# Optimization experiments

Hardware: AMD Instinct MI355X
Metric: run time of the kernel (lower is better)

## Reference

```python
import jax, jax.numpy as jnp
import numpy as np

LATENT_N = 1024
COMMITMENT_COST = 1.0
TEMP = 0.1


def setup_inputs() -> dict:
    key = jax.random.key(0)
    k0, k1, k2, k3, k4, k5 = jax.random.split(key, 6)
    N, D, H, Fd, K = 65536, 1024, 128, 512, LATENT_N
    input_data = jax.random.normal(k0, (N, D), dtype=jnp.float32)
    W1 = jax.random.normal(k1, (D, H), dtype=jnp.float32) * (1.0 / np.sqrt(D))
    b1 = jnp.zeros((H,), dtype=jnp.float32)
    W2 = jax.random.normal(k2, (H, Fd), dtype=jnp.float32) * (1.0 / np.sqrt(H))
    b2 = jnp.zeros((Fd,), dtype=jnp.float32)
    code_book = jax.random.uniform(k3, (K, Fd), dtype=jnp.float32,
                                   minval=-1.0 / K, maxval=1.0 / K)
    return {"input_data": input_data, "W1": W1, "b1": b1,
            "W2": W2, "b2": b2, "code_book": code_book}


def reference(input_data, W1, b1, W2, b2, code_book):
    # feat MLP: Linear -> ReLU -> Linear
    z = jnp.matmul(jnp.maximum(jnp.matmul(input_data, W1) + b1, 0.0), W2) + b2  # [N, F]
    # squared L2 distances to codebook entries: [N, K]
    distances = (jnp.sum(z * z, axis=1, keepdims=True)
                 + jnp.sum(code_book * code_book, axis=1)
                 - 2.0 * jnp.matmul(z, code_book.T))
    logits = -distances / TEMP
    # categorical sample per row (softmax of logits)
    idx = jax.random.categorical(jax.random.key(42), logits, axis=-1)  # [N] int
    encodings = jax.nn.one_hot(idx, LATENT_N, dtype=z.dtype)  # [N, K]
    quantized = jnp.matmul(encodings, code_book)  # [N, F] == code_book[idx]
    e_latent_loss = jnp.mean((jax.lax.stop_gradient(quantized) - z) ** 2)
    q_latent_loss = jnp.mean((quantized - jax.lax.stop_gradient(z)) ** 2)
    loss = q_latent_loss + COMMITMENT_COST * e_latent_loss
    # straight-through estimator
    quantized_st = z + jax.lax.stop_gradient(quantized - z)
    avg_probs = jnp.mean(encodings, axis=0)  # [K]
    perplexity = jnp.exp(-jnp.sum(avg_probs * jnp.log(avg_probs + 1e-10)))
    return (loss, quantized_st, perplexity, encodings, -distances)
```

## Files before the change

### kernel.cpp

```cpp
#include <hip/hip_runtime.h>
#include <stdint.h>

#define N_ROWS 65536
#define DIM 1024
#define HID 128
#define FD 512
#define KCB 1024
#define HALFCNT 33554432u

#define OFF_Q    1
#define OFF_PERP 33554433
#define OFF_ENC  33554434
#define OFF_ND   100663298

typedef __attribute__((ext_vector_type(8))) short sh8;
typedef __attribute__((ext_vector_type(4))) float f32x4;

__device__ __forceinline__ uint32_t rotl32(uint32_t v, int r) { return (v << r) | (v >> (32 - r)); }

__device__ __forceinline__ void threefry(uint32_t c0, uint32_t c1, uint32_t& o0, uint32_t& o1) {
    const uint32_t ks0 = 0u, ks1 = 42u, ks2 = 0x1BD11BDAu ^ 0u ^ 42u;
    uint32_t x0 = c0 + ks0, x1 = c1 + ks1;
#define TFR(r) x0 += x1; x1 = rotl32(x1, r); x1 ^= x0;
    TFR(13) TFR(15) TFR(26) TFR(6)  x0 += ks1; x1 += ks2 + 1u;
    TFR(17) TFR(29) TFR(16) TFR(24) x0 += ks2; x1 += ks0 + 2u;
    TFR(13) TFR(15) TFR(26) TFR(6)  x0 += ks0; x1 += ks1 + 3u;
    TFR(17) TFR(29) TFR(16) TFR(24) x0 += ks1; x1 += ks2 + 4u;
    TFR(13) TFR(15) TFR(26) TFR(6)  x0 += ks2; x1 += ks0 + 5u;
#undef TFR
    o0 = x0; o1 = x1;
}

__device__ __forceinline__ float gumbel_f32(uint32_t b) {
    uint32_t m = b >> 9;
    float u = m ? (float)m * 1.1920928955078125e-07f : 1.17549435e-38f;
    const float LN2 = 0.6931471805599453f;
    return -LN2 * __log2f(-LN2 * __log2f(u));
}

__device__ __forceinline__ ushort bf16rne(float f) {
    uint32_t u = __float_as_uint(f);
    return (ushort)((u + 0x7FFFu + ((u >> 16) & 1u)) >> 16);
}
__device__ __forceinline__ uint32_t pack2rne(float a, float b) {
    return (uint32_t)bf16rne(a) | ((uint32_t)bf16rne(b) << 16);
}

__device__ __forceinline__ void async_cp16(const void* g, void* l) {
    __builtin_amdgcn_global_load_lds(
        (const __attribute__((address_space(1))) void*)g,
        (__attribute__((address_space(3))) void*)l, 16, 0, 0);
}

__device__ __forceinline__ void nt_store4(float* p, float x, float y, float z, float w) {
    f32x4 v = {x, y, z, w};
    __builtin_nontemporal_store(v, (f32x4*)p);
}

__global__ __launch_bounds__(256) void k_prep(const float* __restrict__ cb, const float* __restrict__ W1,
                                              const float* __restrict__ W2,
                                              ushort* __restrict__ cbh, double* __restrict__ cc,
                                              ushort* __restrict__ w1th, ushort* __restrict__ w2th,
                                              int* __restrict__ counts, double* __restrict__ lossb,
                                              unsigned long long* __restrict__ wkey) {
    int gb = blockIdx.x, t = threadIdx.x;
    if (gb < 256) {
        int k = gb * 4 + (t >> 6), l = t & 63;
        const float4* row = (const float4*)(cb + (size_t)k * FD);
        float4 a = row[l * 2], b = row[l * 2 + 1];
        float v[8] = {a.x, a.y, a.z, a.w, b.x, b.y, b.z, b.w};
        double s = 0.0;
        uint32_t hu[4];
        #pragma unroll
        for (int e = 0; e < 4; ++e) {
            hu[e] = pack2rne(v[2 * e], v[2 * e + 1]);
            s = fma((double)v[2 * e], (double)v[2 * e], s);
            s = fma((double)v[2 * e + 1], (double)v[2 * e + 1], s);
        }
        *(uint4*)(cbh + (size_t)k * FD + l * 8) = make_uint4(hu[0], hu[1], hu[2], hu[3]);
        for (int off = 32; off; off >>= 1) s += __shfl_down(s, off, 64);
        if (l == 0) cc[k] = s;
    } else if (gb < 384) {
        int c = gb - 256;
        #pragma unroll
        for (int u = 0; u < 4; ++u) {
            int k = t + u * 256;
            w1th[(size_t)c * DIM + k] = bf16rne(W1[(size_t)k * HID + c]);
        }
    } else if (gb < 640) {
        int c = (gb - 384) * 2 + (t >> 7);
        int tt = t & 127;
        w2th[(size_t)c * HID + tt] = bf16rne(W2[(size_t)tt * FD + c]);
    } else if (gb == 640) {
        for (int k = t; k < KCB; k += 256) counts[k] = 0;
        lossb[t] = 0.0;
    } else {
        unsigned long long* p = wkey + (size_t)(gb - 641) * 2048;
        #pragma unroll
        for (int u = 0; u < 8; ++u) p[t + u * 256] = 0ull;
    }
}

__global__ __launch_bounds__(256) void kAB(const float* __restrict__ X, const ushort* __restrict__ w1th,
                                           const float* __restrict__ b1, const ushort* __restrict__ w2th,
                                           const float* __restrict__ b2,
                                           ushort* __restrict__ zbh, float* __restrict__ zz) {
    __shared__ __align__(16) char lds[24576];
    __shared__ float zzp[64][2];
    int t = threadIdx.x;
    int lane = t & 63, w = t >> 6;
    int wr = w >> 1, wc = w & 1;
    int lane15 = lane & 15, lg = lane >> 4;
    int n0 = blockIdx.x * 64;
    f32x4 zero4 = {0.f, 0.f, 0.f, 0.f};
    f32x4 acc[2][4];
    #pragma unroll
    for (int i = 0; i < 2; ++i)
        #pragma unroll
        for (int j = 0; j < 4; ++j) acc[i][j] = zero4;

    int xr = t >> 2;
    int cq = (t & 3) * 2;
    int xsw = xr & 7;

    for (int k0 = 0; k0 < DIM; k0 += 64) {
        #pragma unroll
        for (int i = 0; i < 4; ++i) {
            int rr = w * 32 + i * 8;
            int row = rr + (lane >> 3);
            int csrc = (lane & 7) ^ (row & 7);
            async_cp16(w1th + (size_t)row * DIM + k0 + csrc * 8, lds + 8192 + rr * 128);
        }
        const float* xp = X + (size_t)(n0 + xr) * DIM + k0 + cq * 8;
        #pragma unroll
        for (int c = 0; c < 2; ++c) {
            float4 a = *(const float4*)(xp + c * 8);
            float4 b = *(const float4*)(xp + c * 8 + 4);
            uint4 hv;
            hv.x = pack2rne(a.x, a.y);
            hv.y = pack2rne(a.z, a.w);
            hv.z = pack2rne(b.x, b.y);
            hv.w = pack2rne(b.z, b.w);
            *(uint4*)(lds + xr * 128 + (((cq + c) ^ xsw) << 4)) = hv;
        }
        __syncthreads();
        #pragma unroll
        for (int kh = 0; kh < 2; ++kh) {
            int ch = kh * 4 + lg;
            sh8 ah[2], bh[4];
            #pragma unroll
            for (int i = 0; i < 2; ++i) {
                int ra = wr * 32 + i * 16 + lane15;
                ah[i] = *(const sh8*)(lds + ra * 128 + ((ch ^ (ra & 7)) << 4));
            }
            #pragma unroll
            for (int j = 0; j < 4; ++j) {
                int rb = wc * 64 + j * 16 + lane15;
                bh[j] = *(const sh8*)(lds + 8192 + rb * 128 + ((ch ^ (rb & 7)) << 4));
            }
            #pragma unroll
            for (int i = 0; i < 2; ++i)
                #pragma unroll
                for (int j = 0; j < 4; ++j)
                    acc[i][j] = __builtin_amdgcn_mfma_f32_16x16x32_bf16(ah[i], bh[j], acc[i][j], 0, 0, 0);
        }
        __syncthreads();
    }
    #pragma unroll
    for (int j = 0; j < 4; ++j) {
        int hcol = wc * 64 + j * 16 + lane15;
        float b1v = b1[hcol];
        int k8 = hcol >> 3, klo = hcol & 7;
        #pragma unroll
        for (int i = 0; i < 2; ++i)
            #pragma unroll
            for (int r = 0; r < 4; ++r) {
                int row = wr * 32 + i * 16 + lg * 4 + r;
                ushort hb = bf16rne(fmaxf(acc[i][j][r] + b1v, 0.f));
                *(ushort*)(lds + row * 256 + ((k8 ^ (row & 7)) << 4) + klo * 2) = hb;
            }
    }
    __syncthreads();
    float zsum[8];
    #pragma unroll
    for (int e = 0; e < 8; ++e) zsum[e] = 0.f;
    for (int c2 = 0; c2 < 4; ++c2) {
        f32x4 acc2[2][4];
        #pragma unroll
        for (int i = 0; i < 2; ++i)
            #pragma unroll
            for (int j = 0; j < 4; ++j) acc2[i][j] = zero4;
        #pragma unroll
        for (int kh = 0; kh < 4; ++kh) {
            int ch = kh * 4 + lg;
            sh8 ah[2], bh[4];
            #pragma unroll
            for (int i = 0; i < 2; ++i) {
                int ra = wr * 32 + i * 16 + lane15;
                ah[i] = *(const sh8*)(lds + ra * 256 + ((ch ^ (ra & 7)) << 4));
            }
            #pragma unroll
            for (int j = 0; j < 4; ++j) {
                int col = c2 * 128 + wc * 64 + j * 16 + lane15;
                bh[j] = *(const sh8*)(w2th + (size_t)col * HID + ch * 8);
            }
            #pragma unroll
            for (int i = 0; i < 2; ++i)
                #pragma unroll
                for (int j = 0; j < 4; ++j)
                    acc2[i][j] = __builtin_amdgcn_mfma_f32_16x16x32_bf16(ah[i], bh[j], acc2[i][j], 0, 0, 0);
        }
        #pragma unroll
        for (int j = 0; j < 4; ++j) {
            int col = c2 * 128 + wc * 64 + j * 16 + lane15;
            float b2v = b2[col];
            #pragma unroll
            for (int i = 0; i < 2; ++i)
                #pragma unroll
                for (int r = 0; r < 4; ++r) {
                    int row = wr * 32 + i * 16 + lg * 4 + r;
                    float v = acc2[i][j][r] + b2v;
                    zbh[(size_t)(n0 + row) * FD + col] = bf16rne(v);
                    zsum[i * 4 + r] = fmaf(v, v, zsum[i * 4 + r]);
                }
        }
    }
    #pragma unroll
    for (int e = 0; e < 8; ++e) {
        float s = zsum[e];
        s += __shfl_xor(s, 1, 64); s += __shfl_xor(s, 2, 64);
        s += __shfl_xor(s, 4, 64); s += __shfl_xor(s, 8, 64);
        if (lane15 == 0) zzp[wr * 32 + (e >> 2) * 16 + lg * 4 + (e & 3)][wc] = s;
    }
    __syncthreads();
    if (t < 64) zz[n0 + t] = zzp[t][0] + zzp[t][1];
}

__global__ __launch_bounds__(256) void k_mfma3p(const ushort* __restrict__ zbh, const ushort* __restrict__ cbh,
                                                const float* __restrict__ zz, const double* __restrict__ cc,
                                                float* __restrict__ nd,
                                                unsigned long long* __restrict__ wkey) {
    __shared__ __align__(16) char lds[32768];
    int t = threadIdx.x;
    int lane = t & 63, w = t >> 6;
    int wr = w >> 1, wc = w & 1;
    int bid = blockIdx.x;
    int pm = ((bid >> 6) << 3) | (bid & 7);
    int bkn = (bid >> 3) & 7;
    const ushort* Bhg = cbh + (size_t)bkn * 128 * FD;

    f32x4 zero4 = {0.f, 0.f, 0.f, 0.f};
    f32x4 acc[4][4];
    #pragma unroll
    for (int i = 0; i < 4; ++i)
        #pragma unroll
        for (int j = 0; j < 4; ++j) acc[i][j] = zero4;

    for (int k0 = 0; k0 < FD; k0 += 64) {
        #pragma unroll
        for (int i = 0; i < 4; ++i) {
            int rr = w * 32 + i * 8;
            int row = rr + (lane >> 3);
            int csrc = (lane & 7) ^ (row & 7);
            int ga = pm * 64 + (row >> 6) * 32 + (row & 31) + (((row >> 5) & 1) ? 32768 : 0);
            async_cp16(zbh + (size_t)ga * FD + k0 + csrc * 8, lds + rr * 128);
            async_cp16(Bhg + (size_t)row * FD + k0 + csrc * 8, lds + 16384 + rr * 128);
        }
        __syncthreads();
        #pragma unroll
        for (int kh = 0; kh < 2; ++kh) {
            int ch = kh * 4 + (lane >> 4);
            sh8 ah[4], bh[4];
            #pragma unroll
            for (int i = 0; i < 4; ++i) {
                int ra = wr * 64 + i * 16 + (lane & 15);
                ah[i] = *(const sh8*)(lds + ra * 128 + ((ch ^ (ra & 7)) << 4));
            }
            #pragma unroll
            for (int j = 0; j < 4; ++j) {
                int rb = wc * 64 + j * 16 + (lane & 15);
                bh[j] = *(const sh8*)(lds + 16384 + rb * 128 + ((ch ^ (rb & 7)) << 4));
            }
            #pragma unroll
            for (int i = 0; i < 4; ++i)
                #pragma unroll
                for (int j = 0; j < 4; ++j)
                    acc[i][j] = __builtin_amdgcn_mfma_f32_16x16x32_bf16(ah[i], bh[j], acc[i][j], 0, 0, 0);
        }
        __syncthreads();
    }
    int lane15 = lane & 15, lg = lane >> 4;
    int gcol[4];
    double ccv[4];
    #pragma unroll
    for (int j = 0; j < 4; ++j) {
        gcol[j] = bkn * 128 + wc * 64 + j * 16 + lane15;
        ccv[j] = cc[gcol[j]];
    }
    #pragma unroll
    for (int i2 = 0; i2 < 2; ++i2)
        #pragma unroll
        for (int r = 0; r < 4; ++r) {
            int lowrow = pm * 64 + wr * 32 + i2 * 16 + lg * 4 + r;
            int hirow  = lowrow + 32768;
            float zlo = zz[lowrow], zhi = zz[hirow];
            double zvl = (double)zlo, zvh = (double)zhi;
            size_t rofl = (size_t)lowrow << 10;
            size_t rofh = (size_t)hirow << 10;
            unsigned long long bkl = 0ull, bkh = 0ull;
            #pragma unroll
            for (int j = 0; j < 4; ++j) {
                float ndl = (float)(2.0 * (double)acc[i2][j][r] - zvl - ccv[j]);
                float ndh = (float)(2.0 * (double)acc[i2 + 2][j][r] - zvh - ccv[j]);
                __builtin_nontemporal_store(ndl, nd + rofl + gcol[j]);
                __builtin_nontemporal_store(ndh, nd + rofh + gcol[j]);
                uint32_t base = (uint32_t)lowrow * 1024u + (uint32_t)gcol[j];
                uint32_t r0, r1;
                threefry(base, base + HALFCNT, r0, r1);
                float sl = (ndl + zlo) * 10.0f + gumbel_f32(r0);
                float sh = (ndh + zhi) * 10.0f + gumbel_f32(r1);
                uint32_t ul = __float_as_uint(sl);
                ul ^= (uint32_t)(((int32_t)ul >> 31) | 0x80000000);
                uint32_t uh = __float_as_uint(sh);
                uh ^= (uint32_t)(((int32_t)uh >> 31) | 0x80000000);
                unsigned long long kl = ((unsigned long long)ul << 32) | (uint32_t)(1023 - gcol[j]);
                unsigned long long kh2 = ((unsigned long long)uh << 32) | (uint32_t)(1023 - gcol[j]);
                if (kl > bkl) bkl = kl;
                if (kh2 > bkh) bkh = kh2;
            }
            #pragma unroll
            for (int m = 1; m <= 8; m <<= 1) {
                unsigned long long ol = __shfl_xor(bkl, m, 64);
                unsigned long long oh = __shfl_xor(bkh, m, 64);
                if (ol > bkl) bkl = ol;
                if (oh > bkh) bkh = oh;
            }
            if (lane15 == 0) {
                atomicMax(&wkey[lowrow], bkl);
                atomicMax(&wkey[hirow], bkh);
            }
        }
}

__global__ __launch_bounds__(256) void k_enc2(const unsigned long long* __restrict__ wkey,
                                              const float* __restrict__ nd, const float* __restrict__ cb,
                                              float* __restrict__ enc, float* __restrict__ qz,
                                              int* __restrict__ counts, double* __restrict__ lossb) {
    int t = threadIdx.x;
    int n0 = blockIdx.x * 16;
    __shared__ int si[16];
    if (t < 16) {
        int n = n0 + t;
        unsigned long long best = wkey[n];
        int k = 1023 - (int)(best & 0xFFFFFFFFull);
        si[t] = k;
        atomicAdd(&counts[k], 1);
        float ndv = nd[(size_t)n * KCB + k];
        atomicAdd(&lossb[n & 255], -(double)ndv);
    }
    __syncthreads();
    #pragma unroll
    for (int r = 0; r < 16; ++r) {
        int id = si[r];
        int base = t * 4;
        nt_store4(&enc[(size_t)(n0 + r) * KCB + base],
                  (id == base)     ? 1.0f : 0.0f,
                  (id == base + 1) ? 1.0f : 0.0f,
                  (id == base + 2) ? 1.0f : 0.0f,
                  (id == base + 3) ? 1.0f : 0.0f);
    }
    for (int e = t; e < 16 * 128; e += 256) {
        int r = e >> 7, s = e & 127;
        float4 v = *(const float4*)&cb[(size_t)si[r] * FD + s * 4];
        nt_store4(&qz[(size_t)(n0 + r) * FD + s * 4], v.x, v.y, v.z, v.w);
    }
}

__global__ void k_scalars(const int* __restrict__ counts, const double* __restrict__ lossb,
                          float* __restrict__ out) {
    int t = threadIdx.x;
    double s = 0.0;
    for (int k = t; k < KCB; k += 256) {
        double p = (double)counts[k] * (1.0 / 65536.0);
        s += p * log(p + 1e-10);
    }
    double lsum = lossb[t];
    for (int off = 32; off; off >>= 1) {
        s += __shfl_down(s, off, 64);
        lsum += __shfl_down(lsum, off, 64);
    }
    __shared__ double red[4], redl[4];
    int lane = t & 63, w = t >> 6;
    if (lane == 0) { red[w] = s; redl[w] = lsum; }
    __syncthreads();
    if (t == 0) {
        double tot = red[0] + red[1] + red[2] + red[3];
        double ltot = redl[0] + redl[1] + redl[2] + redl[3];
        out[OFF_PERP] = (float)exp(-tot);
        out[0] = (float)(ltot * (2.0 / 33554432.0));
    }
}

extern "C" void kernel_launch(void* const* d_in, const int* in_sizes, int n_in,
                              void* d_out, int out_size, void* d_ws, size_t ws_size,
                              hipStream_t stream) {
    const float* X  = (const float*)d_in[0];
    const float* W1 = (const float*)d_in[1];
    const float* b1 = (const float*)d_in[2];
    const float* W2 = (const float*)d_in[3];
    const float* b2 = (const float*)d_in[4];
    const float* cb = (const float*)d_in[5];

    float* out = (float*)d_out;
    float* qz  = out + (size_t)OFF_Q;
    float* enc = out + (size_t)OFF_ENC;
    float* nd  = out + (size_t)OFF_ND;

    float* zz = (float*)d_ws;
    double* cc = (double*)(zz + 65536);
    double* lossb = cc + 1024;
    int* counts = (int*)(lossb + 256);
    unsigned long long* wkey = (unsigned long long*)(counts + 1024);

    bool big_ws = ws_size >= ((size_t)100 << 20);
    char* big = big_ws ? ((char*)d_ws + (1 << 20)) : (char*)(enc + 2);
    ushort* ub   = (ushort*)big;
    ushort* zbh  = ub;
    ushort* cbh  = ub + 33554432;
    ushort* w1th = ub + 34078720;
    ushort* w2th = ub + 34209792;

    k_prep<<<673, 256, 0, stream>>>(cb, W1, W2, cbh, cc, w1th, w2th, counts, lossb, wkey);
    kAB<<<1024, 256, 0, stream>>>(X, w1th, b1, w2th, b2, zbh, zz);
    k_mfma3p<<<4096, 256, 0, stream>>>(zbh, cbh, zz, cc, nd, wkey);
    k_enc2<<<4096, 256, 0, stream>>>(wkey, nd, cb, enc, qz, counts, lossb);
    k_scalars<<<1, 256, 0, stream>>>(counts, lossb, out);
}
```

Baseline: 436.4 us.

## Fuse encoding and quantized output into distance kernel via last-block arrival counter

Adds a per-row-group arrival counter so that the last of the eight column blocks covering a group of rows reads the final argmax keys and writes the one-hot encodings, quantized rows, counts and loss terms inside the distance kernel. The separate encoding kernel launch then runs only when the workspace is too small for the fused path. This removes a kernel launch and lets the encoding writes overlap with other blocks' MFMA work, at the cost of atomics, a thread fence, and uneven tail work concentrated in the last-arriving blocks.

```diff
diff --git a/kernel.cpp b/kernel.cpp
--- a/kernel.cpp
+++ b/kernel.cpp
@@ -62,7 +62,8 @@
                                               ushort* __restrict__ cbh, double* __restrict__ cc,
                                               ushort* __restrict__ w1th, ushort* __restrict__ w2th,
                                               int* __restrict__ counts, double* __restrict__ lossb,
-                                              unsigned long long* __restrict__ wkey) {
+                                              unsigned long long* __restrict__ wkey,
+                                              int* __restrict__ arrive) {
     int gb = blockIdx.x, t = threadIdx.x;
     if (gb < 256) {
         int k = gb * 4 + (t >> 6), l = t & 63;
@@ -94,6 +95,8 @@
     } else if (gb == 640) {
         for (int k = t; k < KCB; k += 256) counts[k] = 0;
         lossb[t] = 0.0;
+        arrive[t] = 0;
+        arrive[t + 256] = 0;
     } else {
         unsigned long long* p = wkey + (size_t)(gb - 641) * 2048;
         #pragma unroll
@@ -236,11 +239,17 @@
     if (t < 64) zz[n0 + t] = zzp[t][0] + zzp[t][1];
 }
 
-__global__ __launch_bounds__(256) void k_mfma3p(const ushort* __restrict__ zbh, const ushort* __restrict__ cbh,
+__global__ __launch_bounds__(256) void k_mfma3f(const ushort* __restrict__ zbh, const ushort* __restrict__ cbh,
                                                 const float* __restrict__ zz, const double* __restrict__ cc,
+                                                const float* __restrict__ cbf,
                                                 float* __restrict__ nd,
-                                                unsigned long long* __restrict__ wkey) {
+                                                unsigned long long* __restrict__ wkey,
+                                                int* __restrict__ arrive,
+                                                float* __restrict__ enc, float* __restrict__ qz,
+                                                int* __restrict__ counts, double* __restrict__ lossb,
+                                                int do_inline) {
     __shared__ __align__(16) char lds[32768];
+    __shared__ int lastFlag;
     int t = threadIdx.x;
     int lane = t & 63, w = t >> 6;
     int wr = w >> 1, wc = w & 1;
@@ -340,6 +349,42 @@
                 atomicMax(&wkey[hirow], bkh);
             }
         }
+    if (!do_inline) return;
+    __syncthreads();
+    if (t == 0) {
+        __threadfence();
+        lastFlag = (atomicAdd(&arrive[pm], 1) == 7) ? 1 : 0;
+    }
+    __syncthreads();
+    if (!lastFlag) return;
+    int* sk = (int*)lds;
+    if (t < 128) {
+        int n = pm * 64 + (t & 63) + ((t & 64) ? 32768 : 0);
+        unsigned long long key = atomicMax(&wkey[n], 0ull);
+        int k = 1023 - (int)(key & 0xFFFFFFFFull);
+        sk[t] = k;
+        atomicAdd(&counts[k], 1);
+        float ndv = nd[(size_t)n * KCB + k];
+        atomicAdd(&lossb[n & 255], -(double)ndv);
+    }
+    __syncthreads();
+    #pragma unroll 4
+    for (int r = 0; r < 128; ++r) {
+        int n = pm * 64 + (r & 63) + ((r & 64) ? 32768 : 0);
+        int id = sk[r];
+        int base = t * 4;
+        nt_store4(&enc[(size_t)n * KCB + base],
+                  (id == base)     ? 1.0f : 0.0f,
+                  (id == base + 1) ? 1.0f : 0.0f,
+                  (id == base + 2) ? 1.0f : 0.0f,
+                  (id == base + 3) ? 1.0f : 0.0f);
+    }
+    for (int e = t; e < 128 * 128; e += 256) {
+        int r = e >> 7, s = e & 127;
+        int n = pm * 64 + (r & 63) + ((r & 64) ? 32768 : 0);
+        float4 v = *(const float4*)&cbf[(size_t)sk[r] * FD + s * 4];
+        nt_store4(&qz[(size_t)n * FD + s * 4], v.x, v.y, v.z, v.w);
+    }
 }
 
 __global__ __launch_bounds__(256) void k_enc2(const unsigned long long* __restrict__ wkey,
@@ -421,6 +466,7 @@
     double* lossb = cc + 1024;
     int* counts = (int*)(lossb + 256);
     unsigned long long* wkey = (unsigned long long*)(counts + 1024);
+    int* arrive = (int*)(wkey + 65536);
 
     bool big_ws = ws_size >= ((size_t)100 << 20);
     char* big = big_ws ? ((char*)d_ws + (1 << 20)) : (char*)(enc + 2);
@@ -430,9 +476,10 @@
     ushort* w1th = ub + 34078720;
     ushort* w2th = ub + 34209792;
 
-    k_prep<<<673, 256, 0, stream>>>(cb, W1, W2, cbh, cc, w1th, w2th, counts, lossb, wkey);
+    k_prep<<<673, 256, 0, stream>>>(cb, W1, W2, cbh, cc, w1th, w2th, counts, lossb, wkey, arrive);
     kAB<<<1024, 256, 0, stream>>>(X, w1th, b1, w2th, b2, zbh, zz);
-    k_mfma3p<<<4096, 256, 0, stream>>>(zbh, cbh, zz, cc, nd, wkey);
-    k_enc2<<<4096, 256, 0, stream>>>(wkey, nd, cb, enc, qz, counts, lossb);
+    k_mfma3f<<<4096, 256, 0, stream>>>(zbh, cbh, zz, cc, cb, nd, wkey, arrive,
+                                       enc, qz, counts, lossb, big_ws ? 1 : 0);
+    if (!big_ws) k_enc2<<<4096, 256, 0, stream>>>(wkey, nd, cb, enc, qz, counts, lossb);
     k_scalars<<<1, 256, 0, stream>>>(counts, lossb, out);
 }
```

Result: slower. 723.8 us (+65.9%).
